# Kernel tuning notes

Hardware: AMD Instinct MI355X
Metric: run time of the kernel (lower is better)

## Reference

```python
import jax, jax.numpy as jnp
import numpy as np

N_ITEMS = 50000
N_USERS = 20000
N_NODES = N_ITEMS + N_USERS
D = 128
N_REL = 3
NNZ = 800000
K_LAYERS = 2
B, S, L = 256, 4, 50


def setup_inputs() -> dict:
    key = jax.random.key(0)
    ks = iter(jax.random.split(key, 40))
    stdv = float(1.0 / np.sqrt(D))

    def uni(shape):
        return jax.random.uniform(next(ks), shape, jnp.float32, -stdv, stdv)

    id_emb = (jax.random.normal(next(ks), (N_ITEMS, D), jnp.float32) * 0.1).at[0].set(0.0)  # padding_idx=0
    user_emb = jax.random.normal(next(ks), (N_USERS, D), jnp.float32) * 0.1
    inp = dict(
        id_emb=id_emb, user_emb=user_emb,
        lin_r_w=uni((K_LAYERS, N_REL, D, D)),
        upi_w=uni((K_LAYERS, D, D)), upi_b=uni((K_LAYERS, D)),
        upu_w=uni((K_LAYERS, D, D)), upu_b=uni((K_LAYERS, D)),
        w_ih=uni((3 * D, 2 * D)), w_hh=uni((3 * D, D)),
        b_ih=uni((3 * D,)), b_hh=uni((3 * D,)),
        b_iah=uni((D,)), b_oah=uni((D,)),
        ei_w=uni((D, D)), ei_b=uni((D,)),
        eo_w=uni((D, D)), eo_b=uni((D,)),
        q1_w=uni((D, D)), q2_w=uni((D, D)), att_w=uni((D,)),
        fuse_w=uni((D, 2 * D)), fuse_b=uni((D,)),
    )
    # global heterogeneous graph: COO per relation over item+user nodes
    inp['rel_rows'] = jax.random.randint(next(ks), (N_REL, NNZ), 0, N_NODES, dtype=jnp.int32)
    inp['rel_cols'] = jax.random.randint(next(ks), (N_REL, NNZ), 0, N_NODES, dtype=jnp.int32)
    inp['rel_vals'] = jax.random.uniform(next(ks), (N_REL, NNZ), jnp.float32) * 0.1
    # session batch: every session has length in [2, L]
    lens = jax.random.randint(next(ks), (B, S), 2, L + 1)
    raw = jax.random.randint(next(ks), (B, S, L), 1, N_ITEMS)
    inp['ids'] = (raw * (jnp.arange(L)[None, None, :] < lens[:, :, None])).astype(jnp.int32)
    inp['uid'] = jax.random.randint(next(ks), (B,), 0, N_USERS, dtype=jnp.int32)
    inp['u_type'] = jax.random.randint(next(ks), (B,), 0, 3).astype(jnp.float32)
    return inp


def _hgnn(h_item, h_user, rel_rows, rel_cols, rel_vals, lin_r_w, upi_w, upi_b, upu_w, upu_b):
    Ni = h_item.shape[0]
    N = Ni + h_user.shape[0]
    for k in range(lin_r_w.shape[0]):
        h_all = jnp.concatenate([h_item, h_user], 0)
        msg = jnp.zeros_like(h_all)
        for r in range(rel_rows.shape[0]):
            Wh = h_all @ lin_r_w[k, r].T  # per-relation linear
            msg = msg + jax.ops.segment_sum(Wh[rel_cols[r]] * rel_vals[r][:, None],
                                            rel_rows[r], num_segments=N)  # sparse.mm
        h_item = jax.nn.relu((msg[:Ni] + h_item) @ upi_w[k].T + upi_b[k])
        h_user = jax.nn.relu((msg[Ni:] + h_user) @ upu_w[k].T + upu_b[k])
    return h_item, h_user


def reference(id_emb, user_emb, lin_r_w, upi_w, upi_b, upu_w, upu_b,
              w_ih, w_hh, b_ih, b_hh, b_iah, b_oah,
              ei_w, ei_b, eo_w, eo_b, q1_w, q2_w, att_w, fuse_w, fuse_b,
              rel_rows, rel_cols, rel_vals, ids, uid, u_type):
    Bb, Ss, Ll = ids.shape
    N = Ss * Bb
    ids_sb = jnp.transpose(ids, (1, 0, 2)).reshape(N, Ll)  # session-major, matches torch concat order
    lens = (ids_sb != 0).sum(-1)  # >= 2 by construction -> all sessions valid
    rows = jnp.arange(N)
    target = ids_sb[rows, lens - 1]
    Lp = Ll - 1
    m_in = jnp.arange(Lp)[None, :] < (lens - 1)[:, None]
    seq_in = ids_sb[:, :Lp] * m_in
    # session graph: consecutive-item edges; in-half sub-diagonal, out-half super-diagonal
    valid = (m_in[:, 1:] & m_in[:, :-1]).astype(jnp.float32)  # [N, Lp-1]
    i1 = jnp.arange(1, Lp)
    i0 = jnp.arange(Lp - 1)
    a_in = jnp.zeros((N, Lp, Lp), jnp.float32).at[:, i1, i0].set(valid)
    a_out = jnp.zeros((N, Lp, Lp), jnp.float32).at[:, i0, i1].set(valid)
    deg = jnp.clip(a_in.sum(-1), 1.0, None)[..., None]
    a_in = a_in / deg
    a_out = a_out / deg
    h = id_emb[seq_in]  # [N, Lp, D]
    # SessionGNN GRU-style cell (step=1)
    m_i = jnp.matmul(a_in, h @ ei_w.T + ei_b) + b_iah
    m_o = jnp.matmul(a_out, h @ eo_w.T + eo_b) + b_oah
    gi = jnp.concatenate([m_i, m_o], -1) @ w_ih.T + b_ih
    gh = h @ w_hh.T + b_hh
    i_r, i_i, i_n = jnp.split(gi, 3, -1)
    h_r, h_i, h_n = jnp.split(gh, 3, -1)
    rg = jax.nn.sigmoid(i_r + h_r)
    zg = jax.nn.sigmoid(i_i + h_i)
    ng = jnp.tanh(i_n + rg * h_n)
    h = ng + zg * (h - ng)
    # attention readout
    ht = h[rows, jnp.clip(lens - 2, 0, None)]
    alpha = jax.nn.sigmoid((ht @ q1_w.T)[:, None, :] + h @ q2_w.T) @ att_w  # [N, Lp]
    alpha = alpha * m_in.astype(jnp.float32)
    alpha = alpha / (alpha.sum(1, keepdims=True) + 1e-8)
    c_cur = jnp.einsum('nl,nld->nd', alpha, h)
    # global HGNN user context
    g_item, g_user = _hgnn(id_emb[:N_ITEMS], user_emb[:N_USERS], rel_rows, rel_cols,
                           rel_vals, lin_r_w, upi_w, upi_b, upu_w, upu_b)
    c_hist = g_user[jnp.tile(uid, Ss)]
    reps = jnp.concatenate([c_cur, c_hist], -1) @ fuse_w.T + fuse_b
    return reps, target, jnp.tile(u_type, Ss)
```

## Files before the change

### kernel.cpp

```cpp
#include <hip/hip_runtime.h>
#include <hip/hip_bf16.h>

typedef __hip_bfloat16 bf16;
typedef unsigned int uint32;
typedef __attribute__((ext_vector_type(8))) short short8;
typedef __attribute__((ext_vector_type(4))) float f32x4;
typedef __attribute__((ext_vector_type(2))) float f32x2;
typedef __attribute__((ext_vector_type(4))) uint32 u32x4;

#define N_ITEMS_C 50000
#define N_USERS_C 20000
#define N_NODES_C 70000
#define NNZ_C 800000
#define NSESS 1024
#define LP 49
#define NTOK (NSESS * LP)
#define NBK 137

__device__ __forceinline__ float bflo(uint32 u) { return __uint_as_float(u << 16); }
__device__ __forceinline__ float bfhi(uint32 u) { return __uint_as_float(u & 0xffff0000u); }
__device__ __forceinline__ float bfhi_fast(uint32 u) { return __uint_as_float(u); }
__device__ __forceinline__ uint32 packbf(float a, float b) {
    return (uint32)__bfloat16_as_ushort(__float2bfloat16(a)) |
           ((uint32)__bfloat16_as_ushort(__float2bfloat16(b)) << 16);
}

__global__ void init_hab_kernel(const float2* __restrict__ idp, const float2* __restrict__ usp,
                                uint32* __restrict__ hab) {
    int i = blockIdx.x * 256 + threadIdx.x;
    float2 w = (i < 3200000) ? idp[i] : usp[i - 3200000];
    hab[i] = packbf(w.x, w.y);
}

__global__ __launch_bounds__(256) void bucket_hist_kernel(
    const int* __restrict__ rel_rows, int* __restrict__ bhist)
{
    __shared__ int hist[NBK];
    const int r = blockIdx.y, tid = threadIdx.x;
    if (tid < NBK) hist[tid] = 0;
    __syncthreads();
    const int* rr = rel_rows + (size_t)r * NNZ_C;
#pragma unroll
    for (int i = 0; i < 16; ++i) {
        int e = blockIdx.x * 4096 + i * 256 + tid;
        if (e < NNZ_C) atomicAdd(&hist[rr[e] >> 9], 1);
    }
    __syncthreads();
    if (tid < NBK && hist[tid]) atomicAdd(&bhist[r * NBK + tid], hist[tid]);
}

__global__ __launch_bounds__(256) void bucket_scan_kernel(
    const int* __restrict__ bhist, int* __restrict__ bbase)
{
    __shared__ int s[256];
    const int tid = threadIdx.x;
    for (int r = 0; r < 3; ++r) {
        s[tid] = (tid < NBK) ? bhist[r * NBK + tid] : 0;
        __syncthreads();
        for (int d = 1; d < 256; d <<= 1) {
            int t = (tid >= d) ? s[tid - d] : 0;
            __syncthreads();
            s[tid] += t;
            __syncthreads();
        }
        if (tid < NBK) bbase[r * (NBK + 1) + tid + 1] = s[tid];
        if (tid == 0) bbase[r * (NBK + 1)] = 0;
        __syncthreads();
    }
}

__global__ __launch_bounds__(256) void bucket_scatter_kernel(
    const int* __restrict__ rel_rows, const int* __restrict__ rel_cols,
    const float* __restrict__ rel_vals, const int* __restrict__ bbase,
    int* __restrict__ cursor, int2* __restrict__ tmp)
{
    __shared__ int hist[NBK], gbase[NBK], cur2[NBK];
    const int r = blockIdx.y, tid = threadIdx.x;
    if (tid < NBK) { hist[tid] = 0; cur2[tid] = 0; }
    __syncthreads();
    const int* rr = rel_rows + (size_t)r * NNZ_C;
    const int* rc = rel_cols + (size_t)r * NNZ_C;
    const float* rv = rel_vals + (size_t)r * NNZ_C;
#pragma unroll
    for (int i = 0; i < 16; ++i) {
        int e = blockIdx.x * 4096 + i * 256 + tid;
        if (e < NNZ_C) atomicAdd(&hist[rr[e] >> 9], 1);
    }
    __syncthreads();
    if (tid < NBK)
        gbase[tid] = bbase[r * (NBK + 1) + tid] +
                     (hist[tid] ? atomicAdd(&cursor[r * NBK + tid], hist[tid]) : 0);
    __syncthreads();
    int2* tp = tmp + (size_t)r * NNZ_C;
#pragma unroll
    for (int i = 0; i < 16; ++i) {
        int e = blockIdx.x * 4096 + i * 256 + tid;
        if (e < NNZ_C) {
            int row = rr[e];
            int bk = row >> 9;
            int rank = atomicAdd(&cur2[bk], 1);
            uint32 fb = __float_as_uint(rv[e]);
            uint32 pk = (uint32)rc[e] | (((fb >> 16) & 0x7FFFu) << 17);
            tp[gbase[bk] + rank] = make_int2((int)pk, row);
        }
    }
}

__global__ __launch_bounds__(256) void bucket_refine_kernel(
    const int2* __restrict__ tmp, const int* __restrict__ bbase,
    int* __restrict__ offs, uint32* __restrict__ edges)
{
    __shared__ int cnt[512], offsL[512], cur[512];
    __shared__ uint32 outb[6656];
    const int b = blockIdx.x, r = blockIdx.y, tid = threadIdx.x;
    const int lane = tid & 63, wid = tid >> 6;
    const int row0 = b << 9;
    const int e0 = bbase[r * (NBK + 1) + b];
    const int e1 = bbase[r * (NBK + 1) + b + 1];
    cnt[tid] = 0; cnt[256 + tid] = 0; cur[tid] = 0; cur[256 + tid] = 0;
    __syncthreads();
    const int2* tp = tmp + (size_t)r * NNZ_C;
    for (int e = e0 + tid; e < e1; e += 256)
        atomicAdd(&cnt[tp[e].y - row0], 1);
    __syncthreads();
    if (wid == 0) {
        int carry = 0;
        for (int c = 0; c < 8; ++c) {
            int x = cnt[c * 64 + lane];
            int inc = x;
#pragma unroll
            for (int d = 1; d < 64; d <<= 1) {
                int y = __shfl_up(inc, d, 64);
                if (lane >= d) inc += y;
            }
            offsL[c * 64 + lane] = inc - x + carry;
            carry += __shfl(inc, 63, 64);
        }
    }
    __syncthreads();
    for (int i = tid; i < 512; i += 256) {
        int row = row0 + i;
        if (row < 70001) offs[(size_t)r * 70001 + row] = e0 + offsL[i];
    }
    for (int e = e0 + tid; e < e1; e += 256) {
        int2 E = tp[e];
        int lr_ = E.y - row0;
        int slot = offsL[lr_] + atomicAdd(&cur[lr_], 1);
        if (slot < 6656) outb[slot] = (uint32)E.x;
    }
    __syncthreads();
    uint32* eo = edges + (size_t)r * NNZ_C + e0;
    for (int i = tid; i < e1 - e0; i += 256) eo[i] = outb[i];
}

__global__ __launch_bounds__(256) void gather_kernel(
    const uint32* __restrict__ hab, const uint32* __restrict__ edges,
    const int* __restrict__ offs, uint32* __restrict__ T)
{
    const int row = blockIdx.x * 4 + (threadIdx.x >> 6);
    const int lane = threadIdx.x & 63;
    const int grp = lane >> 4;
    const int ql  = lane & 15;
    const char* __restrict__ habB = (const char*)hab + ql * 16;
    f32x2 acc[3][4];
#pragma unroll
    for (int r = 0; r < 3; ++r)
#pragma unroll
        for (int j = 0; j < 4; ++j) acc[r][j] = (f32x2){0.f, 0.f};
#pragma unroll
    for (int r = 0; r < 3; ++r) {
        const uint32* __restrict__ ed = edges + (size_t)r * NNZ_C;
        const int* __restrict__ of = offs + (size_t)r * 70001;
        const int e0 = of[row], e1 = of[row + 1];
        if (e0 >= e1) continue;
        const uint32 span = (uint32)(e1 - e0);
        const int s0 = e0 & ~3;
        for (int eb = s0; eb < e1; eb += 16) {
            const int base = eb + grp * 4;
            uint4 E4 = *(const uint4*)&ed[base];
            uint32 Ej0 = ((uint32)(base + 0 - e0) < span) ? E4.x : 0u;
            uint32 Ej1 = ((uint32)(base + 1 - e0) < span) ? E4.y : 0u;
            uint32 Ej2 = ((uint32)(base + 2 - e0) < span) ? E4.z : 0u;
            uint32 Ej3 = ((uint32)(base + 3 - e0) < span) ? E4.w : 0u;
            uint4 u0 = *(const uint4*)(habB + ((Ej0 & 0x1FFFFu) << 8));
            uint4 u1 = *(const uint4*)(habB + ((Ej1 & 0x1FFFFu) << 8));
            uint4 u2 = *(const uint4*)(habB + ((Ej2 & 0x1FFFFu) << 8));
            uint4 u3 = *(const uint4*)(habB + ((Ej3 & 0x1FFFFu) << 8));
            float v0 = __uint_as_float((Ej0 >> 1) & 0x7FFF0000u);
            float v1 = __uint_as_float((Ej1 >> 1) & 0x7FFF0000u);
            float v2 = __uint_as_float((Ej2 >> 1) & 0x7FFF0000u);
            float v3 = __uint_as_float((Ej3 >> 1) & 0x7FFF0000u);
            f32x2 vv;
            vv = (f32x2){v0, v0};
            acc[r][0] += vv * (f32x2){bflo(u0.x), bfhi_fast(u0.x)};
            acc[r][1] += vv * (f32x2){bflo(u0.y), bfhi_fast(u0.y)};
            acc[r][2] += vv * (f32x2){bflo(u0.z), bfhi_fast(u0.z)};
            acc[r][3] += vv * (f32x2){bflo(u0.w), bfhi_fast(u0.w)};
            vv = (f32x2){v1, v1};
            acc[r][0] += vv * (f32x2){bflo(u1.x), bfhi_fast(u1.x)};
            acc[r][1] += vv * (f32x2){bflo(u1.y), bfhi_fast(u1.y)};
            acc[r][2] += vv * (f32x2){bflo(u1.z), bfhi_fast(u1.z)};
            acc[r][3] += vv * (f32x2){bflo(u1.w), bfhi_fast(u1.w)};
            vv = (f32x2){v2, v2};
            acc[r][0] += vv * (f32x2){bflo(u2.x), bfhi_fast(u2.x)};
            acc[r][1] += vv * (f32x2){bflo(u2.y), bfhi_fast(u2.y)};
            acc[r][2] += vv * (f32x2){bflo(u2.z), bfhi_fast(u2.z)};
            acc[r][3] += vv * (f32x2){bflo(u2.w), bfhi_fast(u2.w)};
            vv = (f32x2){v3, v3};
            acc[r][0] += vv * (f32x2){bflo(u3.x), bfhi_fast(u3.x)};
            acc[r][1] += vv * (f32x2){bflo(u3.y), bfhi_fast(u3.y)};
            acc[r][2] += vv * (f32x2){bflo(u3.z), bfhi_fast(u3.z)};
            acc[r][3] += vv * (f32x2){bflo(u3.w), bfhi_fast(u3.w)};
        }
    }
    float* af = (float*)acc;
#pragma unroll
    for (int off = 16; off < 64; off <<= 1)
#pragma unroll
        for (int j = 0; j < 24; ++j) af[j] += __shfl_xor(af[j], off, 64);
    if (grp == 0) {
#pragma unroll
        for (int r = 0; r < 3; ++r) {
            u32x4 o;
            o.x = packbf(acc[r][0].x, acc[r][0].y);
            o.y = packbf(acc[r][1].x, acc[r][1].y);
            o.z = packbf(acc[r][2].x, acc[r][2].y);
            o.w = packbf(acc[r][3].x, acc[r][3].y);
            __builtin_nontemporal_store(o, (u32x4*)&T[(size_t)row * 192 + r * 64 + ql * 4]);
        }
    }
}

__global__ __launch_bounds__(256, 3) void wprep_kernel(
    const float* __restrict__ upi_w, const float* __restrict__ upu_w,
    const float* __restrict__ lin_r_w, int k, uint32* __restrict__ Wcat)
{
    __shared__ float As[128][65];
    __shared__ __align__(8) bf16 Ws[128][66];
    const int which = blockIdx.y, seg = which / 3, r = which % 3;
    const float* U  = (seg == 0 ? upi_w : upu_w) + (size_t)k * 16384;
    const float* Wr = lin_r_w + (size_t)(k * 3 + r) * 16384;
    uint32* out = Wcat + (size_t)seg * 32768;
    const int tid = threadIdx.x;
    const int row0 = blockIdx.x * 64;
#pragma unroll
    for (int i = 0; i < 8; ++i) {
        int id = i * 256 + tid;
        int rr = id >> 5, c4 = (id & 31) << 2;
        float4 v = *(const float4*)&U[(size_t)(row0 + rr) * 128 + c4];
        As[c4][rr] = v.x; As[c4+1][rr] = v.y; As[c4+2][rr] = v.z; As[c4+3][rr] = v.w;
    }
    const int m0 = (tid & 15) * 4;
    const int n0 = (tid >> 4) * 8;
    float acc[4][8];
#pragma unroll
    for (int i = 0; i < 4; ++i)
#pragma unroll
        for (int j = 0; j < 8; ++j) acc[i][j] = 0.f;
    for (int p = 0; p < 2; ++p) {
        if (p) __syncthreads();
        for (int i = 0; i < 32; ++i) {
            int id = i * 256 + tid;
            int c = id >> 6, kf = id & 63;
            Ws[c][kf] = __float2bfloat16(Wr[(size_t)(p * 64 + kf) * 128 + c]);
        }
        __syncthreads();
        for (int k2 = 0; k2 < 32; ++k2) {
            int kk = p * 64 + 2 * k2;
            float av0[4], av1[4];
#pragma unroll
            for (int i = 0; i < 4; ++i) { av0[i] = As[kk][m0 + i]; av1[i] = As[kk + 1][m0 + i]; }
#pragma unroll
            for (int j = 0; j < 8; ++j) {
                uint32 wp = *(const uint32*)&Ws[n0 + j][2 * k2];
                float w0 = bflo(wp), w1 = bfhi(wp);
#pragma unroll
                for (int i = 0; i < 4; ++i)
                    acc[i][j] = fmaf(av1[i], w1, fmaf(av0[i], w0, acc[i][j]));
            }
        }
    }
#pragma unroll
    for (int i = 0; i < 4; ++i) {
        int n = row0 + m0 + i;
#pragma unroll
        for (int j = 0; j < 8; j += 2)
            out[(size_t)n * 256 + (r * 128 + n0 + j) / 2] = packbf(acc[i][j], acc[i][j + 1]);
    }
}

__global__ __launch_bounds__(256) void upack_kernel(
    const float* __restrict__ upi_w, const float* __restrict__ upu_w,
    int k, uint32* __restrict__ Wcat)
{
    int id = blockIdx.x * 256 + threadIdx.x;
    int seg = id >> 13, p = id & 8191;
    int n = p >> 6, j2 = (p & 63);
    const float* U = (seg ? upu_w : upi_w) + (size_t)k * 16384;
    float2 w = *(const float2*)&U[(size_t)n * 128 + j2 * 2];
    Wcat[(size_t)seg * 32768 + (size_t)n * 256 + 192 + j2] = packbf(w.x, w.y);
}

__global__ __launch_bounds__(256) void hgnn_update_mfma_kernel(
    const bf16* __restrict__ T, uint32* __restrict__ hab,
    const bf16* __restrict__ Wcat, const float* __restrict__ bias, int row0, int M)
{
    const int tid = threadIdx.x;
    const int wv = tid >> 6, lane = tid & 63, quad = lane >> 4, lr = lane & 15;
    const int rbase = blockIdx.x * 64;
    const bf16* hb = (const bf16*)hab;
    f32x4 acc[4][2];
#pragma unroll
    for (int mt = 0; mt < 4; ++mt) { acc[mt][0] = (f32x4){0,0,0,0}; acc[mt][1] = (f32x4){0,0,0,0}; }
    int arow[4];
#pragma unroll
    for (int mt = 0; mt < 4; ++mt) {
        int rr = rbase + mt * 16 + lr;
        arow[mt] = row0 + (rr < M ? rr : M - 1);
    }
#pragma unroll
    for (int ks = 0; ks < 16; ++ks) {
        short8 b0 = *(const short8*)&Wcat[(size_t)(wv * 32 + lr) * 512 + ks * 32 + quad * 8];
        short8 b1 = *(const short8*)&Wcat[(size_t)(wv * 32 + 16 + lr) * 512 + ks * 32 + quad * 8];
#pragma unroll
        for (int mt = 0; mt < 4; ++mt) {
            short8 a;
            if (ks < 12) a = *(const short8*)&T[(size_t)arow[mt] * 384 + ks * 32 + quad * 8];
            else         a = *(const short8*)&hb[(size_t)arow[mt] * 128 + (ks - 12) * 32 + quad * 8];
            acc[mt][0] = __builtin_amdgcn_mfma_f32_16x16x32_bf16(a, b0, acc[mt][0], 0, 0, 0);
            acc[mt][1] = __builtin_amdgcn_mfma_f32_16x16x32_bf16(a, b1, acc[mt][1], 0, 0, 0);
        }
    }
    __syncthreads();
    unsigned short* hw = (unsigned short*)hab;
#pragma unroll
    for (int s = 0; s < 2; ++s) {
        int col = wv * 32 + s * 16 + lr;
        float bv = bias[col];
#pragma unroll
        for (int mt = 0; mt < 4; ++mt)
#pragma unroll
            for (int reg = 0; reg < 4; ++reg) {
                int rr = rbase + mt * 16 + quad * 4 + reg;
                if (rr < M) {
                    float v = fmaxf(acc[mt][s][reg] + bv, 0.f);
                    hw[(size_t)(row0 + rr) * 128 + col] = __bfloat16_as_ushort(__float2bfloat16(v));
                }
            }
    }
}

__global__ __launch_bounds__(256) void mfma_nt_kernel(
    const bf16* __restrict__ A, const int* __restrict__ rowmap,
    const bf16* __restrict__ W0, const bf16* __restrict__ W1,
    const float* __restrict__ b0, const float* __restrict__ b1,
    float* __restrict__ O0, float* __restrict__ O1, int M)
{
    const int tid = threadIdx.x;
    const int wv = tid >> 6, lane = tid & 63, quad = lane >> 4, lr = lane & 15;
    const int rbase = blockIdx.x * 64;
    int arow[4];
#pragma unroll
    for (int mt = 0; mt < 4; ++mt) {
        int rr = rbase + mt * 16 + lr;
        rr = rr < M ? rr : M - 1;
        arow[mt] = rowmap ? rowmap[rr] : rr;
    }
    f32x4 acc0[4][2], acc1[4][2];
#pragma unroll
    for (int mt = 0; mt < 4; ++mt) {
        acc0[mt][0] = (f32x4){0,0,0,0}; acc0[mt][1] = (f32x4){0,0,0,0};
        acc1[mt][0] = (f32x4){0,0,0,0}; acc1[mt][1] = (f32x4){0,0,0,0};
    }
#pragma unroll
    for (int ks = 0; ks < 4; ++ks) {
        short8 b00 = *(const short8*)&W0[(size_t)(wv * 32 + lr) * 128 + ks * 32 + quad * 8];
        short8 b01 = *(const short8*)&W0[(size_t)(wv * 32 + 16 + lr) * 128 + ks * 32 + quad * 8];
        short8 b10, b11;
        if (W1) {
            b10 = *(const short8*)&W1[(size_t)(wv * 32 + lr) * 128 + ks * 32 + quad * 8];
            b11 = *(const short8*)&W1[(size_t)(wv * 32 + 16 + lr) * 128 + ks * 32 + quad * 8];
        }
#pragma unroll
        for (int mt = 0; mt < 4; ++mt) {
            short8 a = *(const short8*)&A[(size_t)arow[mt] * 128 + ks * 32 + quad * 8];
            acc0[mt][0] = __builtin_amdgcn_mfma_f32_16x16x32_bf16(a, b00, acc0[mt][0], 0, 0, 0);
            acc0[mt][1] = __builtin_amdgcn_mfma_f32_16x16x32_bf16(a, b01, acc0[mt][1], 0, 0, 0);
            if (W1) {
                acc1[mt][0] = __builtin_amdgcn_mfma_f32_16x16x32_bf16(a, b10, acc1[mt][0], 0, 0, 0);
                acc1[mt][1] = __builtin_amdgcn_mfma_f32_16x16x32_bf16(a, b11, acc1[mt][1], 0, 0, 0);
            }
        }
    }
#pragma unroll
    for (int s = 0; s < 2; ++s) {
        int col = wv * 32 + s * 16 + lr;
        float bv0 = b0 ? b0[col] : 0.f;
        float bv1 = (W1 && b1) ? b1[col] : 0.f;
#pragma unroll
        for (int mt = 0; mt < 4; ++mt)
#pragma unroll
            for (int reg = 0; reg < 4; ++reg) {
                int rr = rbase + mt * 16 + quad * 4 + reg;
                if (rr < M) {
                    O0[(size_t)rr * 128 + col] = acc0[mt][s][reg] + bv0;
                    if (W1) O1[(size_t)rr * 128 + col] = acc1[mt][s][reg] + bv1;
                }
            }
    }
}

__global__ void session_prep_kernel(const int* __restrict__ ids, const int* __restrict__ uid,
                                    const float* __restrict__ u_type,
                                    int* __restrict__ lens, int* __restrict__ rowmap,
                                    float* __restrict__ out_target, float* __restrict__ out_utype)
{
    int n = blockIdx.x * 256 + threadIdx.x;
    if (n >= NSESS) return;
    int b = n & 255, s = n >> 8;
    const int* row = ids + (size_t)(b * 4 + s) * 50;
    int len = 0;
#pragma unroll
    for (int l = 0; l < 50; ++l) len += (row[l] != 0) ? 1 : 0;
    lens[n] = len;
    rowmap[n] = n * LP + (len - 2);
    out_target[n] = (float)row[len - 1];
    out_utype[n] = u_type[b];
}

__global__ void chist_kernel(const uint32* __restrict__ hab, const int* __restrict__ uid,
                             float* __restrict__ chist) {
    int n = blockIdx.x, d = threadIdx.x;
    uint32 u = hab[(size_t)(N_ITEMS_C + uid[n & 255]) * 64 + (d >> 1)];
    chist[(size_t)n * 128 + d] = (d & 1) ? bfhi(u) : bflo(u);
}

__global__ void h0_gather_kernel(const float* __restrict__ id_emb, const int* __restrict__ ids,
                                 const int* __restrict__ lens, uint32* __restrict__ hb) {
    int g = blockIdx.x, d = threadIdx.x;
    int n = g / LP;
    int tt = g - n * LP;
    int len = lens[n];
    int b = n & 255, s = n >> 8;
    int id = (tt < len - 1) ? ids[(size_t)(b * 4 + s) * 50 + tt] : 0;
    float2 e = *(const float2*)&id_emb[(size_t)id * 128 + d * 2];
    hb[(size_t)g * 64 + d] = packbf(e.x, e.y);
}

__global__ __launch_bounds__(256) void epack_kernel(
    const float* __restrict__ w_ih, const float* __restrict__ w_hh,
    const float* __restrict__ ei_w, const float* __restrict__ eo_w,
    const float* __restrict__ q2_w, const float* __restrict__ q1_w,
    uint32* __restrict__ dst)
{
    int id = blockIdx.x * 256 + threadIdx.x;
    const float* src; int off;
    if      (id <  49152) { src = w_ih; off = id; }
    else if (id <  73728) { src = w_hh; off = id - 49152; }
    else if (id <  81920) { src = ei_w; off = id - 73728; }
    else if (id <  90112) { src = eo_w; off = id - 81920; }
    else if (id <  98304) { src = q2_w; off = id - 90112; }
    else                  { src = q1_w; off = id - 98304; }
    float2 w = *(const float2*)&src[(size_t)off * 2];
    dst[id] = packbf(w.x, w.y);
}

__global__ __launch_bounds__(256, 2) void gru_mfma_kernel(
    const float* __restrict__ hEi, const float* __restrict__ hEo,
    uint32* __restrict__ hb, const int* __restrict__ lens,
    const bf16* __restrict__ wihb,
    const bf16* __restrict__ whhb,
    const float* __restrict__ b_ih, const float* __restrict__ b_hh,
    const float* __restrict__ b_iah, const float* __restrict__ b_oah)
{
    __shared__ __align__(16) bf16 Agi[64][264];
    __shared__ __align__(16) bf16 Agh[64][136];
    const int tid = threadIdx.x;
    const int g0 = blockIdx.x * 64;

#pragma unroll 4
    for (int i = 0; i < 32; ++i) {
        int p = i * 256 + tid;
        int row = p >> 7, kp = p & 127;
        int g = g0 + row;
        int n = g / LP;
        int tt = g - n * LP;
        int len = lens[n];
        int kk = (kp & 63) * 2;
        float v0, v1;
        if (kp < 64) {
            v0 = b_iah[kk]; v1 = b_iah[kk + 1];
            if (tt >= 1 && tt < len - 1) {
                float2 e = *(const float2*)&hEi[(size_t)(g - 1) * 128 + kk];
                v0 += e.x; v1 += e.y;
            }
        } else {
            v0 = b_oah[kk]; v1 = b_oah[kk + 1];
            if (tt < len - 2) {
                float2 e = *(const float2*)&hEo[(size_t)(g + 1) * 128 + kk];
                v0 += e.x; v1 += e.y;
            }
        }
        *(uint32*)&Agi[row][kp * 2] = packbf(v0, v1);
    }
#pragma unroll 4
    for (int i = 0; i < 16; ++i) {
        int p = i * 256 + tid;
        int row = p >> 6, kp = p & 63;
        *(uint32*)&Agh[row][kp * 2] = hb[(size_t)(g0 + row) * 64 + kp];
    }
    __syncthreads();

    const int wv = tid >> 6;
    const int lane = tid & 63;
    const int quad = lane >> 4;
    const int lr = lane & 15;
    const int c0 = wv * 32;

    f32x4 acc[4][2][4];
#pragma unroll
    for (int mt = 0; mt < 4; ++mt)
#pragma unroll
        for (int s = 0; s < 2; ++s)
#pragma unroll
            for (int j = 0; j < 4; ++j) acc[mt][s][j] = (f32x4){0.f, 0.f, 0.f, 0.f};

#pragma unroll 2
    for (int ks = 0; ks < 8; ++ks) {
        short8 bfr[2][3];
#pragma unroll
        for (int s = 0; s < 2; ++s)
#pragma unroll
            for (int gte = 0; gte < 3; ++gte) {
                int n0 = gte * 128 + c0 + s * 16 + lr;
                bfr[s][gte] = *(const short8*)&wihb[(size_t)n0 * 256 + ks * 32 + quad * 8];
            }
#pragma unroll
        for (int mt = 0; mt < 4; ++mt) {
            short8 a = *(const short8*)&Agi[mt * 16 + lr][ks * 32 + quad * 8];
#pragma unroll
            for (int s = 0; s < 2; ++s) {
                acc[mt][s][0] = __builtin_amdgcn_mfma_f32_16x16x32_bf16(a, bfr[s][0], acc[mt][s][0], 0, 0, 0);
                acc[mt][s][1] = __builtin_amdgcn_mfma_f32_16x16x32_bf16(a, bfr[s][1], acc[mt][s][1], 0, 0, 0);
                acc[mt][s][2] = __builtin_amdgcn_mfma_f32_16x16x32_bf16(a, bfr[s][2], acc[mt][s][2], 0, 0, 0);
            }
        }
    }
#pragma unroll 2
    for (int ks = 0; ks < 4; ++ks) {
        short8 bfr[2][3];
#pragma unroll
        for (int s = 0; s < 2; ++s)
#pragma unroll
            for (int gte = 0; gte < 3; ++gte) {
                int n0 = gte * 128 + c0 + s * 16 + lr;
                bfr[s][gte] = *(const short8*)&whhb[(size_t)n0 * 128 + ks * 32 + quad * 8];
            }
#pragma unroll
        for (int mt = 0; mt < 4; ++mt) {
            short8 a = *(const short8*)&Agh[mt * 16 + lr][ks * 32 + quad * 8];
#pragma unroll
            for (int s = 0; s < 2; ++s) {
                acc[mt][s][0] = __builtin_amdgcn_mfma_f32_16x16x32_bf16(a, bfr[s][0], acc[mt][s][0], 0, 0, 0);
                acc[mt][s][1] = __builtin_amdgcn_mfma_f32_16x16x32_bf16(a, bfr[s][1], acc[mt][s][1], 0, 0, 0);
                acc[mt][s][3] = __builtin_amdgcn_mfma_f32_16x16x32_bf16(a, bfr[s][2], acc[mt][s][3], 0, 0, 0);
            }
        }
    }

    unsigned short* hu = (unsigned short*)hb;
#pragma unroll
    for (int s = 0; s < 2; ++s) {
        int col = c0 + s * 16 + lr;
        float brz = b_ih[col] + b_hh[col];
        float bzz = b_ih[col + 128] + b_hh[col + 128];
        float bin = b_ih[col + 256];
        float bhn = b_hh[col + 256];
#pragma unroll
        for (int mt = 0; mt < 4; ++mt)
#pragma unroll
            for (int reg = 0; reg < 4; ++reg) {
                int row = g0 + mt * 16 + quad * 4 + reg;
                float rg = 1.f / (1.f + expf(-(acc[mt][s][0][reg] + brz)));
                float zg = 1.f / (1.f + expf(-(acc[mt][s][1][reg] + bzz)));
                float ng = tanhf(acc[mt][s][2][reg] + bin + rg * (acc[mt][s][3][reg] + bhn));
                size_t idx = (size_t)row * 128 + col;
                float ho = __uint_as_float((uint32)hu[idx] << 16);
                hu[idx] = __bfloat16_as_ushort(__float2bfloat16(ng + zg * (ho - ng)));
            }
    }
}

__global__ __launch_bounds__(128) void attn_fuse_kernel(
    const float* __restrict__ q1h, const float* __restrict__ q2h,
    const unsigned short* __restrict__ hu, const float* __restrict__ chist,
    const int* __restrict__ lens, const float* __restrict__ att_w,
    const float* __restrict__ fuse_w, const float* __restrict__ fuse_b,
    float* __restrict__ out)
{
    __shared__ float q1s[128], aws[128], al[64], cv[256];
    const int n = blockIdx.x, tid = threadIdx.x;
    q1s[tid] = q1h[(size_t)n * 128 + tid];
    aws[tid] = att_w[tid];
    if (tid < 64) al[tid] = 0.f;
    __syncthreads();
    const int len = lens[n];
    if (tid < len - 1) {
        const float* q2 = &q2h[(size_t)(n * LP + tid) * 128];
        float s = 0.f;
        for (int d = 0; d < 128; ++d) {
            float x = q1s[d] + q2[d];
            s += aws[d] / (1.f + expf(-x));
        }
        al[tid] = s;
    }
    __syncthreads();
    float ssum = 0.f;
    for (int t = 0; t < len - 1; ++t) ssum += al[t];
    float inv = 1.f / (ssum + 1e-8f);
    float c = 0.f;
    for (int t = 0; t < len - 1; ++t) {
        float hv = __uint_as_float((uint32)hu[(size_t)(n * LP + t) * 128 + tid] << 16);
        c += al[t] * inv * hv;
    }
    cv[tid] = c;
    cv[128 + tid] = chist[(size_t)n * 128 + tid];
    __syncthreads();
    float s = fuse_b[tid];
    const float* fr = fuse_w + (size_t)tid * 256;
    for (int k = 0; k < 256; ++k) s += cv[k] * fr[k];
    out[(size_t)n * 128 + tid] = s;
}

extern "C" void kernel_launch(void* const* d_in, const int* in_sizes, int n_in,
                              void* d_out, int out_size, void* d_ws, size_t ws_size,
                              hipStream_t stream)
{
    const float* id_emb   = (const float*)d_in[0];
    const float* user_emb = (const float*)d_in[1];
    const float* lin_r_w  = (const float*)d_in[2];
    const float* upi_w    = (const float*)d_in[3];
    const float* upi_b    = (const float*)d_in[4];
    const float* upu_w    = (const float*)d_in[5];
    const float* upu_b    = (const float*)d_in[6];
    const float* w_ih     = (const float*)d_in[7];
    const float* w_hh     = (const float*)d_in[8];
    const float* b_ih     = (const float*)d_in[9];
    const float* b_hh     = (const float*)d_in[10];
    const float* b_iah    = (const float*)d_in[11];
    const float* b_oah    = (const float*)d_in[12];
    const float* ei_w     = (const float*)d_in[13];
    const float* ei_b     = (const float*)d_in[14];
    const float* eo_w     = (const float*)d_in[15];
    const float* eo_b     = (const float*)d_in[16];
    const float* q1_w     = (const float*)d_in[17];
    const float* q2_w     = (const float*)d_in[18];
    const float* att_w    = (const float*)d_in[19];
    const float* fuse_w   = (const float*)d_in[20];
    const float* fuse_b   = (const float*)d_in[21];
    const int*  rel_rows  = (const int*)d_in[22];
    const int*  rel_cols  = (const int*)d_in[23];
    const float* rel_vals = (const float*)d_in[24];
    const int*  ids       = (const int*)d_in[25];
    const int*  uid       = (const int*)d_in[26];
    const float* u_type   = (const float*)d_in[27];
    float* out = (float*)d_out;

    uint32* W32    = (uint32*)d_ws;
    uint32* hab    = W32;
    uint32* T      = W32 + 4480000;
    uint32* edges  = W32 + 17920000;
    int2*   tmp    = (int2*)(W32 + 20320000);
    int*    offs   = (int*)(W32 + 25120000);
    int*    bhist  = (int*)(W32 + 25330004);
    int*    cursor = (int*)(W32 + 25330415);
    int*    bbase  = (int*)(W32 + 25330826);
    uint32* Wcat   = W32 + 25331240;
    float*  q1h    = (float*)(W32 + 25396776);
    float*  chist  = (float*)(W32 + 25527848);
    int*    lens   = (int*)(W32 + 25658920);
    int*    rowmap = (int*)(W32 + 25659944);
    uint32* sess_hb = W32;
    float* sess_Ei  = (float*)(W32 + 4480000);
    float* sess_Eo  = (float*)(W32 + 10902528);
    float* q2h      = sess_Ei;
    uint32* wpk     = W32 + 17920000;
    uint32* wihb = wpk;
    uint32* whhb = wpk + 49152;
    uint32* eiwb = wpk + 73728;
    uint32* eowb = wpk + 81920;
    uint32* q2wb = wpk + 90112;
    uint32* q1wb = wpk + 98304;
    if (ws_size < (size_t)27144192 * 4 + 4096) return;

    init_hab_kernel<<<17500, 256, 0, stream>>>((const float2*)id_emb, (const float2*)user_emb, hab);
    hipMemsetAsync(bhist, 0, (size_t)822 * 4, stream);
    bucket_hist_kernel<<<dim3(196, 3), 256, 0, stream>>>(rel_rows, bhist);
    bucket_scan_kernel<<<1, 256, 0, stream>>>(bhist, bbase);
    bucket_scatter_kernel<<<dim3(196, 3), 256, 0, stream>>>(rel_rows, rel_cols, rel_vals,
                                                            bbase, cursor, tmp);
    bucket_refine_kernel<<<dim3(NBK, 3), 256, 0, stream>>>(tmp, bbase, offs, edges);

    for (int k = 0; k < 2; ++k) {
        wprep_kernel<<<dim3(2, 6), 256, 0, stream>>>(upi_w, upu_w, lin_r_w, k, Wcat);
        upack_kernel<<<64, 256, 0, stream>>>(upi_w, upu_w, k, Wcat);
        gather_kernel<<<17500, 256, 0, stream>>>(hab, edges, offs, T);
        hgnn_update_mfma_kernel<<<782, 256, 0, stream>>>((const bf16*)T, hab,
            (const bf16*)Wcat, upi_b + k * 128, 0, N_ITEMS_C);
        hgnn_update_mfma_kernel<<<313, 256, 0, stream>>>((const bf16*)T, hab,
            (const bf16*)(Wcat + 32768), upu_b + k * 128, N_ITEMS_C, N_USERS_C);
    }

    session_prep_kernel<<<4, 256, 0, stream>>>(ids, uid, u_type, lens, rowmap,
        out + 131072, out + 132096);
    chist_kernel<<<NSESS, 128, 0, stream>>>(hab, uid, chist);
    epack_kernel<<<416, 256, 0, stream>>>(w_ih, w_hh, ei_w, eo_w, q2_w, q1_w, wpk);
    h0_gather_kernel<<<NTOK, 64, 0, stream>>>(id_emb, ids, lens, sess_hb);
    mfma_nt_kernel<<<784, 256, 0, stream>>>((const bf16*)sess_hb, nullptr,
        (const bf16*)eiwb, (const bf16*)eowb, ei_b, eo_b, sess_Ei, sess_Eo, NTOK);
    gru_mfma_kernel<<<NTOK / 64, 256, 0, stream>>>(sess_Ei, sess_Eo, sess_hb, lens,
        (const bf16*)wihb, (const bf16*)whhb, b_ih, b_hh, b_iah, b_oah);
    mfma_nt_kernel<<<784, 256, 0, stream>>>((const bf16*)sess_hb, nullptr,
        (const bf16*)q2wb, nullptr, nullptr, nullptr, q2h, nullptr, NTOK);
    mfma_nt_kernel<<<16, 256, 0, stream>>>((const bf16*)sess_hb, rowmap,
        (const bf16*)q1wb, nullptr, nullptr, nullptr, q1h, nullptr, NSESS);
    attn_fuse_kernel<<<NSESS, 128, 0, stream>>>(q1h, q2h, (const unsigned short*)sess_hb,
        chist, lens, att_w, fuse_w, fuse_b, out);
}
```

Measured before the change: 767.8 us.

## Precompute shifted bf16 GRU input matrix and drop LDS staging in GRU kernel

```diff
diff --git a/kernel.cpp b/kernel.cpp
--- a/kernel.cpp
+++ b/kernel.cpp
@@ -410,6 +410,62 @@
     }
 }
 
+__global__ __launch_bounds__(256) void mfma_agi_kernel(
+    const bf16* __restrict__ A,
+    const bf16* __restrict__ Wi, const bf16* __restrict__ Wo,
+    const float* __restrict__ ei_b, const float* __restrict__ eo_b,
+    const float* __restrict__ b_iah, const float* __restrict__ b_oah,
+    const int* __restrict__ lens, unsigned short* __restrict__ AgiG)
+{
+    const int tid = threadIdx.x;
+    const int wv = tid >> 6, lane = tid & 63, quad = lane >> 4, lr = lane & 15;
+    const int rbase = blockIdx.x * 64;
+    int arow[4];
+#pragma unroll
+    for (int mt = 0; mt < 4; ++mt) arow[mt] = rbase + mt * 16 + lr;
+    f32x4 acc0[4][2], acc1[4][2];
+#pragma unroll
+    for (int mt = 0; mt < 4; ++mt) {
+        acc0[mt][0] = (f32x4){0,0,0,0}; acc0[mt][1] = (f32x4){0,0,0,0};
+        acc1[mt][0] = (f32x4){0,0,0,0}; acc1[mt][1] = (f32x4){0,0,0,0};
+    }
+#pragma unroll
+    for (int ks = 0; ks < 4; ++ks) {
+        short8 b00 = *(const short8*)&Wi[(size_t)(wv * 32 + lr) * 128 + ks * 32 + quad * 8];
+        short8 b01 = *(const short8*)&Wi[(size_t)(wv * 32 + 16 + lr) * 128 + ks * 32 + quad * 8];
+        short8 b10 = *(const short8*)&Wo[(size_t)(wv * 32 + lr) * 128 + ks * 32 + quad * 8];
+        short8 b11 = *(const short8*)&Wo[(size_t)(wv * 32 + 16 + lr) * 128 + ks * 32 + quad * 8];
+#pragma unroll
+        for (int mt = 0; mt < 4; ++mt) {
+            short8 a = *(const short8*)&A[(size_t)arow[mt] * 128 + ks * 32 + quad * 8];
+            acc0[mt][0] = __builtin_amdgcn_mfma_f32_16x16x32_bf16(a, b00, acc0[mt][0], 0, 0, 0);
+            acc0[mt][1] = __builtin_amdgcn_mfma_f32_16x16x32_bf16(a, b01, acc0[mt][1], 0, 0, 0);
+            acc1[mt][0] = __builtin_amdgcn_mfma_f32_16x16x32_bf16(a, b10, acc1[mt][0], 0, 0, 0);
+            acc1[mt][1] = __builtin_amdgcn_mfma_f32_16x16x32_bf16(a, b11, acc1[mt][1], 0, 0, 0);
+        }
+    }
+#pragma unroll
+    for (int s = 0; s < 2; ++s) {
+        int col = wv * 32 + s * 16 + lr;
+        float bei = ei_b[col], beo = eo_b[col];
+        float bia = b_iah[col], boa = b_oah[col];
+#pragma unroll
+        for (int mt = 0; mt < 4; ++mt)
+#pragma unroll
+            for (int reg = 0; reg < 4; ++reg) {
+                int rr = rbase + mt * 16 + quad * 4 + reg;
+                int d1 = rr + 1; if (d1 == NTOK) d1 = 0;
+                int n1 = d1 / LP, t1 = d1 - n1 * LP, l1 = lens[n1];
+                float v1 = bia + ((t1 >= 1 && t1 < l1 - 1) ? acc0[mt][s][reg] + bei : 0.f);
+                AgiG[(size_t)d1 * 256 + col] = __bfloat16_as_ushort(__float2bfloat16(v1));
+                int d2 = rr - 1; if (d2 < 0) d2 = NTOK - 1;
+                int n2 = d2 / LP, t2 = d2 - n2 * LP, l2 = lens[n2];
+                float v2 = boa + ((t2 < l2 - 2) ? acc1[mt][s][reg] + beo : 0.f);
+                AgiG[(size_t)d2 * 256 + 128 + col] = __bfloat16_as_ushort(__float2bfloat16(v2));
+            }
+    }
+}
+
 __global__ void session_prep_kernel(const int* __restrict__ ids, const int* __restrict__ uid,
                                     const float* __restrict__ u_type,
                                     int* __restrict__ lens, int* __restrict__ rowmap,
@@ -466,56 +522,22 @@
 }
 
 __global__ __launch_bounds__(256, 2) void gru_mfma_kernel(
-    const float* __restrict__ hEi, const float* __restrict__ hEo,
-    uint32* __restrict__ hb, const int* __restrict__ lens,
+    const bf16* __restrict__ Agi,
+    uint32* __restrict__ hb,
     const bf16* __restrict__ wihb,
     const bf16* __restrict__ whhb,
-    const float* __restrict__ b_ih, const float* __restrict__ b_hh,
-    const float* __restrict__ b_iah, const float* __restrict__ b_oah)
-{
-    __shared__ __align__(16) bf16 Agi[64][264];
-    __shared__ __align__(16) bf16 Agh[64][136];
+    const float* __restrict__ b_ih, const float* __restrict__ b_hh)
+{
     const int tid = threadIdx.x;
-    const int g0 = blockIdx.x * 64;
-
-#pragma unroll 4
-    for (int i = 0; i < 32; ++i) {
-        int p = i * 256 + tid;
-        int row = p >> 7, kp = p & 127;
-        int g = g0 + row;
-        int n = g / LP;
-        int tt = g - n * LP;
-        int len = lens[n];
-        int kk = (kp & 63) * 2;
-        float v0, v1;
-        if (kp < 64) {
-            v0 = b_iah[kk]; v1 = b_iah[kk + 1];
-            if (tt >= 1 && tt < len - 1) {
-                float2 e = *(const float2*)&hEi[(size_t)(g - 1) * 128 + kk];
-                v0 += e.x; v1 += e.y;
-            }
-        } else {
-            v0 = b_oah[kk]; v1 = b_oah[kk + 1];
-            if (tt < len - 2) {
-                float2 e = *(const float2*)&hEo[(size_t)(g + 1) * 128 + kk];
-                v0 += e.x; v1 += e.y;
-            }
-        }
-        *(uint32*)&Agi[row][kp * 2] = packbf(v0, v1);
-    }
-#pragma unroll 4
-    for (int i = 0; i < 16; ++i) {
-        int p = i * 256 + tid;
-        int row = p >> 6, kp = p & 63;
-        *(uint32*)&Agh[row][kp * 2] = hb[(size_t)(g0 + row) * 64 + kp];
-    }
-    __syncthreads();
-
     const int wv = tid >> 6;
     const int lane = tid & 63;
     const int quad = lane >> 4;
     const int lr = lane & 15;
     const int c0 = wv * 32;
+    const int g0 = blockIdx.x * 64;
+    int arow[4];
+#pragma unroll
+    for (int mt = 0; mt < 4; ++mt) arow[mt] = g0 + mt * 16 + lr;
 
     f32x4 acc[4][2][4];
 #pragma unroll
@@ -537,7 +559,7 @@
             }
 #pragma unroll
         for (int mt = 0; mt < 4; ++mt) {
-            short8 a = *(const short8*)&Agi[mt * 16 + lr][ks * 32 + quad * 8];
+            short8 a = *(const short8*)&Agi[(size_t)arow[mt] * 256 + ks * 32 + quad * 8];
 #pragma unroll
             for (int s = 0; s < 2; ++s) {
                 acc[mt][s][0] = __builtin_amdgcn_mfma_f32_16x16x32_bf16(a, bfr[s][0], acc[mt][s][0], 0, 0, 0);
@@ -546,6 +568,7 @@
             }
         }
     }
+    const bf16* hbb = (const bf16*)hb;
 #pragma unroll 2
     for (int ks = 0; ks < 4; ++ks) {
         short8 bfr[2][3];
@@ -558,7 +581,7 @@
             }
 #pragma unroll
         for (int mt = 0; mt < 4; ++mt) {
-            short8 a = *(const short8*)&Agh[mt * 16 + lr][ks * 32 + quad * 8];
+            short8 a = *(const short8*)&hbb[(size_t)arow[mt] * 128 + ks * 32 + quad * 8];
 #pragma unroll
             for (int s = 0; s < 2; ++s) {
                 acc[mt][s][0] = __builtin_amdgcn_mfma_f32_16x16x32_bf16(a, bfr[s][0], acc[mt][s][0], 0, 0, 0);
@@ -568,6 +591,7 @@
         }
     }
 
+    __syncthreads();
     unsigned short* hu = (unsigned short*)hb;
 #pragma unroll
     for (int s = 0; s < 2; ++s) {
@@ -681,9 +705,8 @@
     int*    lens   = (int*)(W32 + 25658920);
     int*    rowmap = (int*)(W32 + 25659944);
     uint32* sess_hb = W32;
-    float* sess_Ei  = (float*)(W32 + 4480000);
-    float* sess_Eo  = (float*)(W32 + 10902528);
-    float* q2h      = sess_Ei;
+    float* q2h      = (float*)(W32 + 4480000);
+    unsigned short* AgiG = (unsigned short*)(W32 + 10902528);
     uint32* wpk     = W32 + 17920000;
     uint32* wihb = wpk;
     uint32* whhb = wpk + 49152;
@@ -716,10 +739,10 @@
     chist_kernel<<<NSESS, 128, 0, stream>>>(hab, uid, chist);
     epack_kernel<<<416, 256, 0, stream>>>(w_ih, w_hh, ei_w, eo_w, q2_w, q1_w, wpk);
     h0_gather_kernel<<<NTOK, 64, 0, stream>>>(id_emb, ids, lens, sess_hb);
-    mfma_nt_kernel<<<784, 256, 0, stream>>>((const bf16*)sess_hb, nullptr,
-        (const bf16*)eiwb, (const bf16*)eowb, ei_b, eo_b, sess_Ei, sess_Eo, NTOK);
-    gru_mfma_kernel<<<NTOK / 64, 256, 0, stream>>>(sess_Ei, sess_Eo, sess_hb, lens,
-        (const bf16*)wihb, (const bf16*)whhb, b_ih, b_hh, b_iah, b_oah);
+    mfma_agi_kernel<<<784, 256, 0, stream>>>((const bf16*)sess_hb,
+        (const bf16*)eiwb, (const bf16*)eowb, ei_b, eo_b, b_iah, b_oah, lens, AgiG);
+    gru_mfma_kernel<<<784, 256, 0, stream>>>((const bf16*)AgiG, sess_hb,
+        (const bf16*)wihb, (const bf16*)whhb, b_ih, b_hh);
     mfma_nt_kernel<<<784, 256, 0, stream>>>((const bf16*)sess_hb, nullptr,
         (const bf16*)q2wb, nullptr, nullptr, nullptr, q2h, nullptr, NTOK);
     mfma_nt_kernel<<<16, 256, 0, stream>>>((const bf16*)sess_hb, rowmap,
```

Measured after the change: 778.5 us. No clear change (+1.4%).
